# Performance work log

Hardware: AMD Instinct MI355X
Metric: run time of the kernel (lower is better)

Reference implementation:

```python
import jax, jax.numpy as jnp
import numpy as np

N, E, W, G = 100000, 625000, 128, 64  # nodes, edges, width, num graphs
EPS = 1e-5


def setup_inputs() -> dict:
    key = jax.random.key(0)
    ks = jax.random.split(key, 8)
    x = jax.random.normal(ks[0], (N, W), jnp.float32)
    edge_index = jax.random.randint(ks[1], (2, E), 0, N, dtype=jnp.int32)
    edge_weight = jax.random.uniform(ks[2], (E,), jnp.float32)
    batch_map = jnp.sort(jax.random.randint(ks[3], (N,), 0, G, dtype=jnp.int32))
    s = 1.0 / np.sqrt(W)
    return {
        "x": x,
        "edge_index": edge_index,
        "edge_weight": edge_weight,
        "batch_map": batch_map,
        "gn_weight": jnp.ones((W,), jnp.float32),
        "gn_bias": jnp.zeros((W,), jnp.float32),
        "gn_mean_scale": jnp.ones((W,), jnp.float32),
        "W_rel1": jax.random.normal(ks[4], (W, W), jnp.float32) * s,
        "b_rel1": jnp.zeros((W,), jnp.float32),
        "W_root1": jax.random.normal(ks[5], (W, W), jnp.float32) * s,
        "W_rel2": jax.random.normal(ks[6], (W, W), jnp.float32) * s,
        "b_rel2": jnp.zeros((W,), jnp.float32),
        "W_root2": jax.random.normal(ks[7], (W, W), jnp.float32) * s,
    }


def _graph_norm(x, batch, weight, bias, mean_scale):
    # per-graph mean / var keyed on batch_map (PyG GraphNorm)
    cnt = jax.ops.segment_sum(jnp.ones((x.shape[0], 1), x.dtype), batch, num_segments=G)
    mean = jax.ops.segment_sum(x, batch, num_segments=G) / cnt
    out = x - mean_scale * mean[batch]
    var = jax.ops.segment_sum(out * out, batch, num_segments=G) / cnt
    std = jnp.sqrt(var + EPS)
    return weight * out / std[batch] + bias


def _graph_conv(x, src, dst, ew, W_rel, b_rel, W_root):
    # out_i = W_rel @ sum_{j->i} e_ji * x_j + b_rel + W_root @ x_i
    msg = x[src] * ew[:, None]                       # [E, W] gather
    agg = jax.ops.segment_sum(msg, dst, num_segments=x.shape[0])  # scatter-add
    return agg @ W_rel.T + b_rel + x @ W_root.T


def reference(x, edge_index, edge_weight, batch_map,
              gn_weight, gn_bias, gn_mean_scale,
              W_rel1, b_rel1, W_root1, W_rel2, b_rel2, W_root2):
    src, dst = edge_index[0], edge_index[1]
    xx = _graph_norm(x, batch_map, gn_weight, gn_bias, gn_mean_scale)
    xx = _graph_conv(xx, src, dst, edge_weight, W_rel1, b_rel1, W_root1)
    xx = jnp.where(xx >= 0, xx, 0.1 * xx)            # LeakyReLU(0.1)
    xx = _graph_conv(xx, src, dst, edge_weight, W_rel2, b_rel2, W_root2)
    return x + xx
```

## Files before the change

### kernel.cpp

```cpp
#include <hip/hip_runtime.h>
#include <hip/hip_bf16.h>

#define WW 128
#define GG 64
#define GN_EPS 1e-5f
#define SCAN_B 1024

typedef __attribute__((ext_vector_type(8))) short short8;
typedef __attribute__((ext_vector_type(4))) float floatx4;

__device__ inline float bf2f(__hip_bfloat16 h) { return __bfloat162float(h); }
__device__ inline float bfbits2f(short v) {
    return __uint_as_float(((unsigned)(unsigned short)v) << 16);
}
__device__ inline short f2bfbits(float f) {
    __hip_bfloat16 h = __float2bfloat16(f);
    return *reinterpret_cast<short*>(&h);
}

__global__ __launch_bounds__(128) void stats_kernel(
    const float* __restrict__ x, const int* __restrict__ batch, int N,
    float* __restrict__ gsum, float* __restrict__ gsumsq, float* __restrict__ gcnt)
{
    int w = threadIdx.x;
    int row0 = blockIdx.x * 32;
    int row1 = min(row0 + 32, N);
    float s = 0.f, ss = 0.f;
    int cur = batch[row0];
    int cnt = 0;
    auto flush = [&]() {
        atomicAdd(&gsum[cur * WW + w], s);
        atomicAdd(&gsumsq[cur * WW + w], ss);
        if (w == 0) atomicAdd(&gcnt[cur], (float)cnt);
        s = 0.f; ss = 0.f; cnt = 0;
    };
    int i = row0;
    for (; i + 4 <= row1; i += 4) {
        int g0 = batch[i + 0], g1 = batch[i + 1], g2 = batch[i + 2], g3 = batch[i + 3];
        float v0 = x[(size_t)(i + 0) * WW + w];
        float v1 = x[(size_t)(i + 1) * WW + w];
        float v2 = x[(size_t)(i + 2) * WW + w];
        float v3 = x[(size_t)(i + 3) * WW + w];
        if (g0 != cur) { flush(); cur = g0; }
        s += v0; ss += v0 * v0; ++cnt;
        if (g1 != cur) { flush(); cur = g1; }
        s += v1; ss += v1 * v1; ++cnt;
        if (g2 != cur) { flush(); cur = g2; }
        s += v2; ss += v2 * v2; ++cnt;
        if (g3 != cur) { flush(); cur = g3; }
        s += v3; ss += v3 * v3; ++cnt;
    }
    for (; i < row1; ++i) {
        int g = batch[i];
        float v = x[(size_t)i * WW + w];
        if (g != cur) { flush(); cur = g; }
        s += v; ss += v * v; ++cnt;
    }
    flush();
}

__global__ __launch_bounds__(256) void finalize_kernel(
    const float* __restrict__ gsum, const float* __restrict__ gsumsq,
    const float* __restrict__ gcnt,
    const float* __restrict__ wgt, const float* __restrict__ bias,
    const float* __restrict__ ms,
    float* __restrict__ scalev, float* __restrict__ shiftv)
{
    int idx = blockIdx.x * blockDim.x + threadIdx.x;
    if (idx >= GG * WW) return;
    int g = idx >> 7, w = idx & (WW - 1);
    float cnt = gcnt[g];
    float inv = cnt > 0.f ? 1.f / cnt : 0.f;
    float mean = gsum[idx] * inv;
    float msw = ms[w];
    float var = gsumsq[idx] * inv - mean * mean * msw * (2.f - msw);
    var = fmaxf(var, 0.f);
    float sc = wgt[w] * rsqrtf(var + GN_EPS);
    scalev[idx] = sc;
    shiftv[idx] = bias[w] - sc * msw * mean;
}

__global__ __launch_bounds__(256) void normalize_kernel(
    const float* __restrict__ x, const int* __restrict__ batch,
    const float* __restrict__ scalev, const float* __restrict__ shiftv,
    __hip_bfloat16* __restrict__ xn, int N)
{
    size_t tid = (size_t)blockIdx.x * blockDim.x + threadIdx.x;
    if (tid >= (size_t)N * (WW / 4)) return;
    int row = (int)(tid >> 5);
    int c4 = (int)(tid & 31) * 4;
    int g = batch[row];
    float4 v = *(const float4*)(x + (size_t)row * WW + c4);
    float4 sc = *(const float4*)(scalev + (size_t)g * WW + c4);
    float4 sh = *(const float4*)(shiftv + (size_t)g * WW + c4);
    __hip_bfloat162 o0, o1;
    o0.x = __float2bfloat16(sc.x * v.x + sh.x);
    o0.y = __float2bfloat16(sc.y * v.y + sh.y);
    o1.x = __float2bfloat16(sc.z * v.z + sh.z);
    o1.y = __float2bfloat16(sc.w * v.w + sh.w);
    union { __hip_bfloat162 h[2]; uint2 u; } pk;
    pk.h[0] = o0; pk.h[1] = o1;
    *(uint2*)(xn + (size_t)row * WW + c4) = pk.u;
}

__global__ __launch_bounds__(256) void cvt_w_kernel(
    const float* __restrict__ w0, const float* __restrict__ w1,
    const float* __restrict__ w2, const float* __restrict__ w3,
    __hip_bfloat16* __restrict__ dst)
{
    int idx = blockIdx.x * blockDim.x + threadIdx.x;
    int m = idx >> 14;
    int o = idx & 16383;
    const float* src = (m == 0) ? w0 : (m == 1) ? w1 : (m == 2) ? w2 : w3;
    dst[idx] = __float2bfloat16(src[o]);
}

__global__ __launch_bounds__(256) void hist_kernel(
    const int* __restrict__ ei, int E, int* __restrict__ deg)
{
    int e = blockIdx.x * 256 + threadIdx.x;
    if (e < E) atomicAdd(&deg[ei[(size_t)E + e]], 1);
}

__global__ __launch_bounds__(SCAN_B) void scan_blocks(
    const int* __restrict__ deg, int N, int* __restrict__ off, int* __restrict__ bsum)
{
    __shared__ int s[SCAN_B];
    int t = threadIdx.x;
    int i = blockIdx.x * SCAN_B + t;
    int v = (i < N) ? deg[i] : 0;
    s[t] = v; __syncthreads();
    for (int d = 1; d < SCAN_B; d <<= 1) {
        int tmp = (t >= d) ? s[t - d] : 0;
        __syncthreads();
        s[t] += tmp;
        __syncthreads();
    }
    if (i < N) off[i] = s[t] - v;
    if (t == SCAN_B - 1) bsum[blockIdx.x] = s[t];
}

__global__ __launch_bounds__(256) void scan_partials(int* __restrict__ bsum, int P)
{
    __shared__ int s[256];
    int t = threadIdx.x;
    int v = (t < P) ? bsum[t] : 0;
    s[t] = v; __syncthreads();
    for (int d = 1; d < 256; d <<= 1) {
        int tmp = (t >= d) ? s[t - d] : 0;
        __syncthreads();
        s[t] += tmp;
        __syncthreads();
    }
    if (t < P) bsum[t] = s[t] - v;
}

__global__ __launch_bounds__(SCAN_B) void add_offsets(
    int* __restrict__ off, const int* __restrict__ bsum, int N)
{
    int i = blockIdx.x * SCAN_B + threadIdx.x;
    if (i < N) off[i] += bsum[blockIdx.x];
}

__global__ __launch_bounds__(256) void place_kernel(
    const int* __restrict__ ei, const float* __restrict__ ew,
    const int* __restrict__ off, int* __restrict__ cursor,
    int2* __restrict__ ebuf, int E)
{
    int base = blockIdx.x * 1024 + threadIdx.x;
    int dstv[4], srcv[4];
    float wv[4];
    int slot[4];
#pragma unroll
    for (int i = 0; i < 4; ++i) {
        int e = base + i * 256;
        dstv[i] = (e < E) ? ei[(size_t)E + e] : -1;
    }
#pragma unroll
    for (int i = 0; i < 4; ++i) {
        int e = base + i * 256;
        if (e < E) { srcv[i] = ei[e]; wv[i] = ew[e]; }
    }
#pragma unroll
    for (int i = 0; i < 4; ++i)
        if (dstv[i] >= 0) slot[i] = off[dstv[i]] + atomicAdd(&cursor[dstv[i]], 1);
#pragma unroll
    for (int i = 0; i < 4; ++i)
        if (dstv[i] >= 0) ebuf[slot[i]] = make_int2(srcv[i], __float_as_int(wv[i]));
}

template <bool OUT_BF16>
__global__ __launch_bounds__(256, 4) void fused_kernel(
    const __hip_bfloat16* __restrict__ X,
    const int2* __restrict__ ebuf, const int* __restrict__ off,
    const int* __restrict__ deg,
    const __hip_bfloat16* __restrict__ Wrel, const __hip_bfloat16* __restrict__ Wroot,
    const float* __restrict__ bias, const float* __restrict__ resid,
    void* __restrict__ outv, int N, int leaky)
{
    __shared__ __align__(16) __hip_bfloat16 smem[2 * 32 * 128];
    __shared__ __align__(16) int2 eshare[512];
    int tid = threadIdx.x;
    int wave = tid >> 6, lane = tid & 63;
    int q = lane >> 4, r16 = lane & 15;
    int rb = blockIdx.x * 32;

#pragma unroll
    for (int s = 0; s < 2; ++s) {
        int t = wave * 2 + s;
        int rloc = t * 4 + (lane >> 4);
        int c = (lane & 15) ^ (rloc & 15);
        int grow = rb + rloc; if (grow >= N) grow = N - 1;
        const __hip_bfloat16* g = X + (size_t)grow * WW + c * 8;
        __hip_bfloat16* l = smem + 4096 + t * 512;
        __builtin_amdgcn_global_load_lds(
            (const __attribute__((address_space(1))) void*)g,
            (__attribute__((address_space(3))) void*)l, 16, 0, 0);
    }

    int endn = min(rb + 32, N) - 1;
    int e0 = off[rb];
    int ne = off[endn] + deg[endn] - e0;
    int nstage = min(ne, 512);
    {
        int pairs = (nstage + 1) >> 1;
        if (tid < pairs) {
            const int2* g = ebuf + e0 + 2 * tid;
            int2* l = eshare + 2 * (wave * 64);
            __builtin_amdgcn_global_load_lds(
                (const __attribute__((address_space(1))) void*)g,
                (__attribute__((address_space(3))) void*)l, 16, 0, 0);
        }
    }
    __syncthreads();

    int node = rb + (tid >> 3);
    int nc = node < N ? node : N - 1;
    int start = off[nc];
    int d = (node < N) ? deg[nc] : 0;
    int lb = start - e0;
    int sub = tid & 7;
    float a16[16];
#pragma unroll
    for (int j = 0; j < 16; ++j) a16[j] = 0.f;
    int last = d - 1;
    for (int k = 0; k <= last; k += 4) {
        int j1 = min(k + 1, last);
        int j2 = min(k + 2, last);
        int j3 = min(k + 3, last);
        int2 p0, p1, p2, p3;
        if (lb + j3 < nstage) {
            p0 = eshare[lb + k];
            p1 = eshare[lb + j1];
            p2 = eshare[lb + j2];
            p3 = eshare[lb + j3];
        } else {
            p0 = (lb + k  < nstage) ? eshare[lb + k]  : ebuf[start + k];
            p1 = (lb + j1 < nstage) ? eshare[lb + j1] : ebuf[start + j1];
            p2 = (lb + j2 < nstage) ? eshare[lb + j2] : ebuf[start + j2];
            p3 = (lb + j3 < nstage) ? eshare[lb + j3] : ebuf[start + j3];
        }
        const __hip_bfloat16* r0 = X + (size_t)p0.x * WW + sub * 16;
        const __hip_bfloat16* r1 = X + (size_t)p1.x * WW + sub * 16;
        const __hip_bfloat16* r2 = X + (size_t)p2.x * WW + sub * 16;
        const __hip_bfloat16* r3 = X + (size_t)p3.x * WW + sub * 16;
        short8 a0 = *(const short8*)(r0);
        short8 b0 = *(const short8*)(r0 + 8);
        short8 a1 = *(const short8*)(r1);
        short8 b1 = *(const short8*)(r1 + 8);
        short8 a2 = *(const short8*)(r2);
        short8 b2 = *(const short8*)(r2 + 8);
        short8 a3 = *(const short8*)(r3);
        short8 b3 = *(const short8*)(r3 + 8);
        float w0 = __int_as_float(p0.y);
        float w1 = (k + 1 <= last) ? __int_as_float(p1.y) : 0.f;
        float w2 = (k + 2 <= last) ? __int_as_float(p2.y) : 0.f;
        float w3 = (k + 3 <= last) ? __int_as_float(p3.y) : 0.f;
#pragma unroll
        for (int j = 0; j < 8; ++j) {
            a16[j]     += w0 * bfbits2f(a0[j]) + w1 * bfbits2f(a1[j]);
            a16[8 + j] += w0 * bfbits2f(b0[j]) + w1 * bfbits2f(b1[j]);
            a16[j]     += w2 * bfbits2f(a2[j]) + w3 * bfbits2f(a3[j]);
            a16[8 + j] += w2 * bfbits2f(b2[j]) + w3 * bfbits2f(b3[j]);
        }
    }

    {
        int r = tid >> 3;
        short8 pk0, pk1;
#pragma unroll
        for (int j = 0; j < 8; ++j) {
            pk0[j] = f2bfbits(a16[j]);
            pk1[j] = f2bfbits(a16[8 + j]);
        }
        int s0 = (2 * sub)     ^ (r & 15);
        int s1 = (2 * sub + 1) ^ (r & 15);
        *(short8*)(smem + r * 128 + s0 * 8) = pk0;
        *(short8*)(smem + r * 128 + s1 * 8) = pk1;
    }

    short8 wf[8][2];
#pragma unroll
    for (int kc = 0; kc < 8; ++kc) {
        const __hip_bfloat16* Wsel = (kc < 4) ? Wrel : Wroot;
        int koff = (kc & 3) * 32 + q * 8;
#pragma unroll
        for (int tt = 0; tt < 2; ++tt) {
            int col = wave * 32 + 2 * r16 + tt;
            wf[kc][tt] = *(const short8*)(Wsel + ((size_t)col * WW + koff));
        }
    }
    float bcol[2];
#pragma unroll
    for (int tt = 0; tt < 2; ++tt) bcol[tt] = bias[wave * 32 + 2 * r16 + tt];

    __syncthreads();

    floatx4 acc[2][2];
#pragma unroll
    for (int r = 0; r < 2; ++r)
#pragma unroll
        for (int tt = 0; tt < 2; ++tt) acc[r][tt] = (floatx4){0.f, 0.f, 0.f, 0.f};

#pragma unroll
    for (int kc = 0; kc < 8; ++kc) {
        int m = kc >> 2;
        short8 af[2];
#pragma unroll
        for (int r = 0; r < 2; ++r) {
            int row = r * 16 + r16;
            int slot = ((kc & 3) * 4 + q) ^ r16;
            af[r] = *(const short8*)(&smem[m * 4096 + row * 128 + slot * 8]);
        }
#pragma unroll
        for (int r = 0; r < 2; ++r) {
            acc[r][0] = __builtin_amdgcn_mfma_f32_16x16x32_bf16(af[r], wf[kc][0], acc[r][0], 0, 0, 0);
            acc[r][1] = __builtin_amdgcn_mfma_f32_16x16x32_bf16(af[r], wf[kc][1], acc[r][1], 0, 0, 0);
        }
    }

    int colb = wave * 32 + 2 * r16;
#pragma unroll
    for (int r = 0; r < 2; ++r)
#pragma unroll
        for (int rr = 0; rr < 4; ++rr) {
            int row = rb + r * 16 + q * 4 + rr;
            if (row < N) {
                float v0 = acc[r][0][rr] + bcol[0];
                float v1 = acc[r][1][rr] + bcol[1];
                if (leaky) {
                    v0 = v0 >= 0.f ? v0 : 0.1f * v0;
                    v1 = v1 >= 0.f ? v1 : 0.1f * v1;
                }
                if (OUT_BF16) {
                    __hip_bfloat162 o;
                    o.x = __float2bfloat16(v0);
                    o.y = __float2bfloat16(v1);
                    *(__hip_bfloat162*)((__hip_bfloat16*)outv + (size_t)row * WW + colb) = o;
                } else {
                    float2 rv = *(const float2*)(resid + (size_t)row * WW + colb);
                    float2 o;
                    o.x = v0 + rv.x;
                    o.y = v1 + rv.y;
                    *(float2*)((float*)outv + (size_t)row * WW + colb) = o;
                }
            }
        }
}

extern "C" void kernel_launch(void* const* d_in, const int* in_sizes, int n_in,
                              void* d_out, int out_size, void* d_ws, size_t ws_size,
                              hipStream_t stream) {
    const float* x      = (const float*)d_in[0];
    const int*   ei     = (const int*)d_in[1];
    const float* ew     = (const float*)d_in[2];
    const int*   batch  = (const int*)d_in[3];
    const float* gnw    = (const float*)d_in[4];
    const float* gnb    = (const float*)d_in[5];
    const float* gnm    = (const float*)d_in[6];
    const float* Wrel1  = (const float*)d_in[7];
    const float* brel1  = (const float*)d_in[8];
    const float* Wroot1 = (const float*)d_in[9];
    const float* Wrel2  = (const float*)d_in[10];
    const float* brel2  = (const float*)d_in[11];
    const float* Wroot2 = (const float*)d_in[12];

    int N = in_sizes[0] / WW;
    int E = in_sizes[1] / 2;
    int P = (N + SCAN_B - 1) / SCAN_B;
    int ntiles = (N + 31) / 32;

    __hip_bfloat16* xn = (__hip_bfloat16*)d_ws;
    __hip_bfloat16* y1 = xn + (size_t)N * WW;
    __hip_bfloat16* Wb = y1 + (size_t)N * WW;
    int2* ebuf   = (int2*)(Wb + 4 * WW * WW);
    int*  deg    = (int*)(ebuf + E);
    int*  cursor = deg + N;
    float* gsum   = (float*)(cursor + N);
    float* gsumsq = gsum + GG * WW;
    float* gcnt   = gsumsq + GG * WW;
    float* scalev = gcnt + GG;
    float* shiftv = scalev + GG * WW;
    int*  off    = (int*)(shiftv + GG * WW);
    int*  bsum   = off + N;

    hipMemsetAsync(deg, 0, ((size_t)2 * N + 2 * GG * WW + GG) * sizeof(int), stream);

    hist_kernel<<<(E + 255) / 256, 256, 0, stream>>>(ei, E, deg);
    scan_blocks<<<P, SCAN_B, 0, stream>>>(deg, N, off, bsum);
    scan_partials<<<1, 256, 0, stream>>>(bsum, P);
    add_offsets<<<P, SCAN_B, 0, stream>>>(off, bsum, N);
    place_kernel<<<(E + 1023) / 1024, 256, 0, stream>>>(ei, ew, off, cursor, ebuf, E);

    cvt_w_kernel<<<(4 * WW * WW) / 256, 256, 0, stream>>>(Wrel1, Wroot1, Wrel2, Wroot2, Wb);
    stats_kernel<<<(N + 31) / 32, 128, 0, stream>>>(x, batch, N, gsum, gsumsq, gcnt);
    finalize_kernel<<<(GG * WW + 255) / 256, 256, 0, stream>>>(
        gsum, gsumsq, gcnt, gnw, gnb, gnm, scalev, shiftv);
    normalize_kernel<<<(int)(((size_t)N * (WW / 4) + 255) / 256), 256, 0, stream>>>(
        x, batch, scalev, shiftv, xn, N);

    fused_kernel<true><<<ntiles, 256, 0, stream>>>(
        xn, ebuf, off, deg, Wb, Wb + WW * WW, brel1, nullptr, y1, N, 1);

    fused_kernel<false><<<ntiles, 256, 0, stream>>>(
        y1, ebuf, off, deg, Wb + 2 * WW * WW, Wb + 3 * WW * WW, brel2, x, d_out, N, 0);
}
```

Measured before the change: 324.0 us.

## Merge preprocessing kernels into fewer launches and widen normalize vectors

Combines the degree histogram, GraphNorm statistics and weight conversion into one launch partitioned by block index. Folds the partial-sum scan into add_offsets by having each block reduce the preceding block sums, and merges edge placement with the GraphNorm finalize step. Normalize now handles 8 columns per thread with 16-byte stores, and the edge buffer is written with nontemporal stores. The aim is fewer kernel launches and serialization gaps, at the cost of redundant per-block reductions and mixed workloads inside one kernel.

```diff
diff --git a/kernel.cpp b/kernel.cpp
--- a/kernel.cpp
+++ b/kernel.cpp
@@ -18,55 +18,151 @@
     return *reinterpret_cast<short*>(&h);
 }
 
-__global__ __launch_bounds__(128) void stats_kernel(
-    const float* __restrict__ x, const int* __restrict__ batch, int N,
-    float* __restrict__ gsum, float* __restrict__ gsumsq, float* __restrict__ gcnt)
-{
-    int w = threadIdx.x;
-    int row0 = blockIdx.x * 32;
-    int row1 = min(row0 + 32, N);
-    float s = 0.f, ss = 0.f;
-    int cur = batch[row0];
-    int cnt = 0;
-    auto flush = [&]() {
-        atomicAdd(&gsum[cur * WW + w], s);
-        atomicAdd(&gsumsq[cur * WW + w], ss);
-        if (w == 0) atomicAdd(&gcnt[cur], (float)cnt);
-        s = 0.f; ss = 0.f; cnt = 0;
-    };
-    int i = row0;
-    for (; i + 4 <= row1; i += 4) {
-        int g0 = batch[i + 0], g1 = batch[i + 1], g2 = batch[i + 2], g3 = batch[i + 3];
-        float v0 = x[(size_t)(i + 0) * WW + w];
-        float v1 = x[(size_t)(i + 1) * WW + w];
-        float v2 = x[(size_t)(i + 2) * WW + w];
-        float v3 = x[(size_t)(i + 3) * WW + w];
-        if (g0 != cur) { flush(); cur = g0; }
-        s += v0; ss += v0 * v0; ++cnt;
-        if (g1 != cur) { flush(); cur = g1; }
-        s += v1; ss += v1 * v1; ++cnt;
-        if (g2 != cur) { flush(); cur = g2; }
-        s += v2; ss += v2 * v2; ++cnt;
-        if (g3 != cur) { flush(); cur = g3; }
-        s += v3; ss += v3 * v3; ++cnt;
-    }
-    for (; i < row1; ++i) {
-        int g = batch[i];
-        float v = x[(size_t)i * WW + w];
-        if (g != cur) { flush(); cur = g; }
-        s += v; ss += v * v; ++cnt;
-    }
-    flush();
-}
-
-__global__ __launch_bounds__(256) void finalize_kernel(
+__global__ __launch_bounds__(256) void prep1_kernel(
+    const int* __restrict__ ei, int E, int* __restrict__ deg, int HB,
+    const float* __restrict__ x, const int* __restrict__ batch, int N, int SB,
+    float* __restrict__ gsum, float* __restrict__ gsumsq, float* __restrict__ gcnt,
+    const float* __restrict__ w0, const float* __restrict__ w1,
+    const float* __restrict__ w2, const float* __restrict__ w3,
+    __hip_bfloat16* __restrict__ wdst)
+{
+    int bid = blockIdx.x;
+    int tid = threadIdx.x;
+
+    if (bid < HB) {
+        int base = bid * 1024 + tid;
+        int d0 = (base             < E) ? ei[(size_t)E + base]       : -1;
+        int d1 = (base + 256       < E) ? ei[(size_t)E + base + 256] : -1;
+        int d2 = (base + 512       < E) ? ei[(size_t)E + base + 512] : -1;
+        int d3 = (base + 768       < E) ? ei[(size_t)E + base + 768] : -1;
+        if (d0 >= 0) atomicAdd(&deg[d0], 1);
+        if (d1 >= 0) atomicAdd(&deg[d1], 1);
+        if (d2 >= 0) atomicAdd(&deg[d2], 1);
+        if (d3 >= 0) atomicAdd(&deg[d3], 1);
+        return;
+    }
+    if (bid < HB + SB) {
+        int sb = bid - HB;
+        int half = tid >> 7;
+        int w = tid & 127;
+        int row0 = sb * 64 + half * 32;
+        if (row0 >= N) return;
+        int row1 = min(row0 + 32, N);
+        float s = 0.f, ss = 0.f;
+        int cur = batch[row0];
+        int cnt = 0;
+        auto flush = [&]() {
+            atomicAdd(&gsum[cur * WW + w], s);
+            atomicAdd(&gsumsq[cur * WW + w], ss);
+            if (w == 0) atomicAdd(&gcnt[cur], (float)cnt);
+            s = 0.f; ss = 0.f; cnt = 0;
+        };
+        int i = row0;
+        for (; i + 4 <= row1; i += 4) {
+            int g0 = batch[i + 0], g1 = batch[i + 1], g2 = batch[i + 2], g3 = batch[i + 3];
+            float v0 = x[(size_t)(i + 0) * WW + w];
+            float v1 = x[(size_t)(i + 1) * WW + w];
+            float v2 = x[(size_t)(i + 2) * WW + w];
+            float v3 = x[(size_t)(i + 3) * WW + w];
+            if (g0 != cur) { flush(); cur = g0; }
+            s += v0; ss += v0 * v0; ++cnt;
+            if (g1 != cur) { flush(); cur = g1; }
+            s += v1; ss += v1 * v1; ++cnt;
+            if (g2 != cur) { flush(); cur = g2; }
+            s += v2; ss += v2 * v2; ++cnt;
+            if (g3 != cur) { flush(); cur = g3; }
+            s += v3; ss += v3 * v3; ++cnt;
+        }
+        for (; i < row1; ++i) {
+            int g = batch[i];
+            float v = x[(size_t)i * WW + w];
+            if (g != cur) { flush(); cur = g; }
+            s += v; ss += v * v; ++cnt;
+        }
+        flush();
+        return;
+    }
+    int idx = (bid - HB - SB) * 256 + tid;
+    int m = idx >> 14;
+    int o = idx & 16383;
+    const float* src = (m == 0) ? w0 : (m == 1) ? w1 : (m == 2) ? w2 : w3;
+    wdst[idx] = __float2bfloat16(src[o]);
+}
+
+__global__ __launch_bounds__(SCAN_B) void scan_blocks(
+    const int* __restrict__ deg, int N, int* __restrict__ off, int* __restrict__ bsum)
+{
+    __shared__ int s[SCAN_B];
+    int t = threadIdx.x;
+    int i = blockIdx.x * SCAN_B + t;
+    int v = (i < N) ? deg[i] : 0;
+    s[t] = v; __syncthreads();
+    for (int d = 1; d < SCAN_B; d <<= 1) {
+        int tmp = (t >= d) ? s[t - d] : 0;
+        __syncthreads();
+        s[t] += tmp;
+        __syncthreads();
+    }
+    if (i < N) off[i] = s[t] - v;
+    if (t == SCAN_B - 1) bsum[blockIdx.x] = s[t];
+}
+
+__global__ __launch_bounds__(SCAN_B) void add_offsets2(
+    int* __restrict__ off, const int* __restrict__ bsum, int N)
+{
+    __shared__ int red[SCAN_B];
+    int t = threadIdx.x;
+    red[t] = (t < blockIdx.x) ? bsum[t] : 0;
+    __syncthreads();
+    for (int s = SCAN_B / 2; s > 0; s >>= 1) {
+        if (t < s) red[t] += red[t + s];
+        __syncthreads();
+    }
+    int i = blockIdx.x * SCAN_B + t;
+    if (i < N) off[i] += red[0];
+}
+
+__global__ __launch_bounds__(256) void place_fin_kernel(
+    const int* __restrict__ ei, const float* __restrict__ ew,
+    const int* __restrict__ off, int* __restrict__ cursor,
+    int2* __restrict__ ebuf, int E, int PB,
     const float* __restrict__ gsum, const float* __restrict__ gsumsq,
     const float* __restrict__ gcnt,
     const float* __restrict__ wgt, const float* __restrict__ bias,
     const float* __restrict__ ms,
     float* __restrict__ scalev, float* __restrict__ shiftv)
 {
-    int idx = blockIdx.x * blockDim.x + threadIdx.x;
+    int bid = blockIdx.x;
+    int tid = threadIdx.x;
+
+    if (bid < PB) {
+        int base = bid * 1024 + tid;
+        int dstv[4], srcv[4];
+        float wv[4];
+        int slot[4];
+#pragma unroll
+        for (int i = 0; i < 4; ++i) {
+            int e = base + i * 256;
+            dstv[i] = (e < E) ? ei[(size_t)E + e] : -1;
+        }
+#pragma unroll
+        for (int i = 0; i < 4; ++i) {
+            int e = base + i * 256;
+            if (e < E) { srcv[i] = ei[e]; wv[i] = ew[e]; }
+        }
+#pragma unroll
+        for (int i = 0; i < 4; ++i)
+            if (dstv[i] >= 0) slot[i] = off[dstv[i]] + atomicAdd(&cursor[dstv[i]], 1);
+#pragma unroll
+        for (int i = 0; i < 4; ++i)
+            if (dstv[i] >= 0) {
+                unsigned long long v = (unsigned)srcv[i]
+                    | ((unsigned long long)__float_as_uint(wv[i]) << 32);
+                __builtin_nontemporal_store(v, (unsigned long long*)&ebuf[slot[i]]);
+            }
+        return;
+    }
+    int idx = (bid - PB) * 256 + tid;
     if (idx >= GG * WW) return;
     int g = idx >> 7, w = idx & (WW - 1);
     float cnt = gcnt[g];
@@ -86,107 +182,29 @@
     __hip_bfloat16* __restrict__ xn, int N)
 {
     size_t tid = (size_t)blockIdx.x * blockDim.x + threadIdx.x;
-    if (tid >= (size_t)N * (WW / 4)) return;
-    int row = (int)(tid >> 5);
-    int c4 = (int)(tid & 31) * 4;
+    if (tid >= (size_t)N * (WW / 8)) return;
+    int row = (int)(tid >> 4);
+    int c8 = (int)(tid & 15) * 8;
     int g = batch[row];
-    float4 v = *(const float4*)(x + (size_t)row * WW + c4);
-    float4 sc = *(const float4*)(scalev + (size_t)g * WW + c4);
-    float4 sh = *(const float4*)(shiftv + (size_t)g * WW + c4);
-    __hip_bfloat162 o0, o1;
-    o0.x = __float2bfloat16(sc.x * v.x + sh.x);
-    o0.y = __float2bfloat16(sc.y * v.y + sh.y);
-    o1.x = __float2bfloat16(sc.z * v.z + sh.z);
-    o1.y = __float2bfloat16(sc.w * v.w + sh.w);
-    union { __hip_bfloat162 h[2]; uint2 u; } pk;
-    pk.h[0] = o0; pk.h[1] = o1;
-    *(uint2*)(xn + (size_t)row * WW + c4) = pk.u;
-}
-
-__global__ __launch_bounds__(256) void cvt_w_kernel(
-    const float* __restrict__ w0, const float* __restrict__ w1,
-    const float* __restrict__ w2, const float* __restrict__ w3,
-    __hip_bfloat16* __restrict__ dst)
-{
-    int idx = blockIdx.x * blockDim.x + threadIdx.x;
-    int m = idx >> 14;
-    int o = idx & 16383;
-    const float* src = (m == 0) ? w0 : (m == 1) ? w1 : (m == 2) ? w2 : w3;
-    dst[idx] = __float2bfloat16(src[o]);
-}
-
-__global__ __launch_bounds__(256) void hist_kernel(
-    const int* __restrict__ ei, int E, int* __restrict__ deg)
-{
-    int e = blockIdx.x * 256 + threadIdx.x;
-    if (e < E) atomicAdd(&deg[ei[(size_t)E + e]], 1);
-}
-
-__global__ __launch_bounds__(SCAN_B) void scan_blocks(
-    const int* __restrict__ deg, int N, int* __restrict__ off, int* __restrict__ bsum)
-{
-    __shared__ int s[SCAN_B];
-    int t = threadIdx.x;
-    int i = blockIdx.x * SCAN_B + t;
-    int v = (i < N) ? deg[i] : 0;
-    s[t] = v; __syncthreads();
-    for (int d = 1; d < SCAN_B; d <<= 1) {
-        int tmp = (t >= d) ? s[t - d] : 0;
-        __syncthreads();
-        s[t] += tmp;
-        __syncthreads();
-    }
-    if (i < N) off[i] = s[t] - v;
-    if (t == SCAN_B - 1) bsum[blockIdx.x] = s[t];
-}
-
-__global__ __launch_bounds__(256) void scan_partials(int* __restrict__ bsum, int P)
-{
-    __shared__ int s[256];
-    int t = threadIdx.x;
-    int v = (t < P) ? bsum[t] : 0;
-    s[t] = v; __syncthreads();
-    for (int d = 1; d < 256; d <<= 1) {
-        int tmp = (t >= d) ? s[t - d] : 0;
-        __syncthreads();
-        s[t] += tmp;
-        __syncthreads();
-    }
-    if (t < P) bsum[t] = s[t] - v;
-}
-
-__global__ __launch_bounds__(SCAN_B) void add_offsets(
-    int* __restrict__ off, const int* __restrict__ bsum, int N)
-{
-    int i = blockIdx.x * SCAN_B + threadIdx.x;
-    if (i < N) off[i] += bsum[blockIdx.x];
-}
-
-__global__ __launch_bounds__(256) void place_kernel(
-    const int* __restrict__ ei, const float* __restrict__ ew,
-    const int* __restrict__ off, int* __restrict__ cursor,
-    int2* __restrict__ ebuf, int E)
-{
-    int base = blockIdx.x * 1024 + threadIdx.x;
-    int dstv[4], srcv[4];
-    float wv[4];
-    int slot[4];
-#pragma unroll
-    for (int i = 0; i < 4; ++i) {
-        int e = base + i * 256;
-        dstv[i] = (e < E) ? ei[(size_t)E + e] : -1;
-    }
-#pragma unroll
-    for (int i = 0; i < 4; ++i) {
-        int e = base + i * 256;
-        if (e < E) { srcv[i] = ei[e]; wv[i] = ew[e]; }
-    }
-#pragma unroll
-    for (int i = 0; i < 4; ++i)
-        if (dstv[i] >= 0) slot[i] = off[dstv[i]] + atomicAdd(&cursor[dstv[i]], 1);
-#pragma unroll
-    for (int i = 0; i < 4; ++i)
-        if (dstv[i] >= 0) ebuf[slot[i]] = make_int2(srcv[i], __float_as_int(wv[i]));
+    const float* xb = x + (size_t)row * WW + c8;
+    const float* scb = scalev + (size_t)g * WW + c8;
+    const float* shb = shiftv + (size_t)g * WW + c8;
+    float4 v0 = *(const float4*)(xb);
+    float4 v1 = *(const float4*)(xb + 4);
+    float4 sc0 = *(const float4*)(scb);
+    float4 sc1 = *(const float4*)(scb + 4);
+    float4 sh0 = *(const float4*)(shb);
+    float4 sh1 = *(const float4*)(shb + 4);
+    union { short s[8]; uint4 u; } pk;
+    pk.s[0] = f2bfbits(sc0.x * v0.x + sh0.x);
+    pk.s[1] = f2bfbits(sc0.y * v0.y + sh0.y);
+    pk.s[2] = f2bfbits(sc0.z * v0.z + sh0.z);
+    pk.s[3] = f2bfbits(sc0.w * v0.w + sh0.w);
+    pk.s[4] = f2bfbits(sc1.x * v1.x + sh1.x);
+    pk.s[5] = f2bfbits(sc1.y * v1.y + sh1.y);
+    pk.s[6] = f2bfbits(sc1.z * v1.z + sh1.z);
+    pk.s[7] = f2bfbits(sc1.w * v1.w + sh1.w);
+    *(uint4*)(xn + (size_t)row * WW + c8) = pk.u;
 }
 
 template <bool OUT_BF16>
@@ -389,6 +407,10 @@
     int E = in_sizes[1] / 2;
     int P = (N + SCAN_B - 1) / SCAN_B;
     int ntiles = (N + 31) / 32;
+    int HB = (E + 1023) / 1024;
+    int SB = (N + 63) / 64;
+    int PB = (E + 1023) / 1024;
+    int FB = (GG * WW + 255) / 256;
 
     __hip_bfloat16* xn = (__hip_bfloat16*)d_ws;
     __hip_bfloat16* y1 = xn + (size_t)N * WW;
@@ -406,17 +428,19 @@
 
     hipMemsetAsync(deg, 0, ((size_t)2 * N + 2 * GG * WW + GG) * sizeof(int), stream);
 
-    hist_kernel<<<(E + 255) / 256, 256, 0, stream>>>(ei, E, deg);
+    prep1_kernel<<<HB + SB + 256, 256, 0, stream>>>(
+        ei, E, deg, HB,
+        x, batch, N, SB, gsum, gsumsq, gcnt,
+        Wrel1, Wroot1, Wrel2, Wroot2, Wb);
+
     scan_blocks<<<P, SCAN_B, 0, stream>>>(deg, N, off, bsum);
-    scan_partials<<<1, 256, 0, stream>>>(bsum, P);
-    add_offsets<<<P, SCAN_B, 0, stream>>>(off, bsum, N);
-    place_kernel<<<(E + 1023) / 1024, 256, 0, stream>>>(ei, ew, off, cursor, ebuf, E);
-
-    cvt_w_kernel<<<(4 * WW * WW) / 256, 256, 0, stream>>>(Wrel1, Wroot1, Wrel2, Wroot2, Wb);
-    stats_kernel<<<(N + 31) / 32, 128, 0, stream>>>(x, batch, N, gsum, gsumsq, gcnt);
-    finalize_kernel<<<(GG * WW + 255) / 256, 256, 0, stream>>>(
+    add_offsets2<<<P, SCAN_B, 0, stream>>>(off, bsum, N);
+
+    place_fin_kernel<<<PB + FB, 256, 0, stream>>>(
+        ei, ew, off, cursor, ebuf, E, PB,
         gsum, gsumsq, gcnt, gnw, gnb, gnm, scalev, shiftv);
-    normalize_kernel<<<(int)(((size_t)N * (WW / 4) + 255) / 256), 256, 0, stream>>>(
+
+    normalize_kernel<<<(int)(((size_t)N * (WW / 8) + 255) / 256), 256, 0, stream>>>(
         x, batch, scalev, shiftv, xn, N);
 
     fused_kernel<true><<<ntiles, 256, 0, stream>>>(
```

Result: faster. 313.7 us (-3.2%).
